# Kernel tuning notes

Measured on AMD Instinct MI355X. Metric: run time of the kernel, lower is better.

The kernel has to match this reference:

```python
import jax, jax.numpy as jnp
import numpy as np

CODEBOOK_SIZE = 512
LATENT_DIM = 12
BATCH = 512
TOKENS = 256


def setup_inputs() -> dict:
    key = jax.random.key(0)
    k1, k2 = jax.random.split(key)
    x = jax.random.normal(k1, (BATCH, TOKENS, LATENT_DIM), dtype=jnp.float32)
    # nn.Embedding init: uniform(-1/K, 1/K)
    lim = 1.0 / CODEBOOK_SIZE
    codebook = jax.random.uniform(k2, (CODEBOOK_SIZE, LATENT_DIM), dtype=jnp.float32,
                                  minval=-lim, maxval=lim)
    return {"x": x, "codebook": codebook}


def reference(x, codebook):
    # same as for torch.cdist (sqrt is monotonic).
    x2 = jnp.sum(x * x, axis=-1, keepdims=True)            # [B, N, 1]
    w2 = jnp.sum(codebook * codebook, axis=-1)             # [K]
    xw = jnp.einsum('bnd,kd->bnk', x, codebook)            # [B, N, K]
    dist2 = x2 - 2.0 * xw + w2                             # [B, N, K]
    indices = jnp.argmin(dist2, axis=-1)                   # [B, N] int
    quantized = codebook[indices]                          # [B, N, D]

    codebook_loss = jnp.mean((quantized - jax.lax.stop_gradient(x)) ** 2)
    commitment_loss = 0.25 * jnp.mean((jax.lax.stop_gradient(quantized) - x) ** 2)
    quantize_loss = codebook_loss + commitment_loss

    # straight-through estimator
    quantized_st = x + jax.lax.stop_gradient(quantized - x)
    return quantized_st, indices, quantize_loss
```

## Files before the change

### kernel.cpp

```cpp
#include <hip/hip_runtime.h>
#include <math.h>

namespace {
constexpr int KCB   = 512;
constexpr int DIM   = 12;
constexpr int NTOK  = 512 * 256;
constexpr int QSIZE = NTOK * DIM;
constexpr int CPL   = 8;
constexpr int TPW   = 32;
constexpr int NWAVE = NTOK / TPW;
constexpr float LSCALE = 1.25f / (float)QSIZE;

__global__ __launch_bounds__(256, 3) void vq_main(const float* __restrict__ x,
                                                  const float* __restrict__ cb,
                                                  float* __restrict__ out,
                                                  float* __restrict__ partials) {
    const int tid  = threadIdx.x;
    const int lane = tid & 63;
    const int wv   = __builtin_amdgcn_readfirstlane(tid >> 6);
    const int wgid = blockIdx.x * 4 + wv;
    const int tb   = wgid * TPW;

    float cw[CPL][DIM];
    float w2[CPL];
#pragma unroll
    for (int j = 0; j < CPL; ++j) {
        const float4* cr = (const float4*)(cb + (size_t)(j * 64 + lane) * DIM);
        float4 c0 = cr[0], c1 = cr[1], c2 = cr[2];
        cw[j][0] = c0.x; cw[j][1] = c0.y; cw[j][2]  = c0.z; cw[j][3]  = c0.w;
        cw[j][4] = c1.x; cw[j][5] = c1.y; cw[j][6]  = c1.z; cw[j][7]  = c1.w;
        cw[j][8] = c2.x; cw[j][9] = c2.y; cw[j][10] = c2.z; cw[j][11] = c2.w;
        float t2 = 0.f;
#pragma unroll
        for (int d = 0; d < DIM; ++d) t2 = fmaf(cw[j][d], cw[j][d], t2);
        w2[j] = t2;
    }

    float losssum = 0.f;
    float idxbuf  = 0.f;

    for (int t = 0; t < TPW; ++t) {
        const float* xr = x + (size_t)(tb + t) * DIM;
        float4 a0 = *(const float4*)(xr + 0);
        float4 a1 = *(const float4*)(xr + 4);
        float4 a2 = *(const float4*)(xr + 8);
        float xv[DIM] = {a0.x, a0.y, a0.z, a0.w, a1.x, a1.y, a1.z, a1.w,
                         a2.x, a2.y, a2.z, a2.w};
        float x2 = 0.f;
#pragma unroll
        for (int d = 0; d < DIM; ++d) x2 = fmaf(xv[d], xv[d], x2);

        float best = INFINITY;
        int   bidx = 0;
        int   kk   = lane;
#pragma unroll
        for (int j = 0; j < CPL; ++j) {
            float xw = 0.f;
            xw = fmaf(xv[0],  cw[j][0],  xw);
            xw = fmaf(xv[1],  cw[j][1],  xw);
            xw = fmaf(xv[2],  cw[j][2],  xw);
            xw = fmaf(xv[3],  cw[j][3],  xw);
            xw = fmaf(xv[4],  cw[j][4],  xw);
            xw = fmaf(xv[5],  cw[j][5],  xw);
            xw = fmaf(xv[6],  cw[j][6],  xw);
            xw = fmaf(xv[7],  cw[j][7],  xw);
            xw = fmaf(xv[8],  cw[j][8],  xw);
            xw = fmaf(xv[9],  cw[j][9],  xw);
            xw = fmaf(xv[10], cw[j][10], xw);
            xw = fmaf(xv[11], cw[j][11], xw);
            float dsc = fmaf(-2.f, xw, x2) + w2[j];
            bool c = dsc < best;
            best = c ? dsc : best;
            bidx = c ? kk : bidx;
            kk += 64;
        }

        float smin = best;
#pragma unroll
        for (int off = 1; off < 64; off <<= 1)
            smin = fminf(smin, __shfl_xor(smin, off));

        unsigned long long mask = __ballot(best == smin);
        int widx;
        if (mask & (mask - 1)) {
            int cand = (best == smin) ? bidx : 0x7fffffff;
#pragma unroll
            for (int off = 1; off < 64; off <<= 1) {
                int o = __shfl_xor(cand, off);
                cand = o < cand ? o : cand;
            }
            widx = cand;
        } else {
            widx = __builtin_amdgcn_readlane(bidx, (int)__builtin_ctzll(mask));
        }

        idxbuf  = (lane == t) ? (float)widx : idxbuf;
        losssum = fmaf(smin, LSCALE, losssum);
    }

    if (lane < TPW) {
        const int t   = tb + lane;
        const int bid = (int)idxbuf;
        const float4* xp = (const float4*)(x + (size_t)t * DIM);
        float4 a0 = xp[0], a1 = xp[1], a2 = xp[2];
        const float4* wr = (const float4*)(cb + (size_t)bid * DIM);
        float4 q0 = wr[0], q1 = wr[1], q2 = wr[2];
        float4 r0, r1, r2;
        r0.x = a0.x + (q0.x - a0.x); r0.y = a0.y + (q0.y - a0.y);
        r0.z = a0.z + (q0.z - a0.z); r0.w = a0.w + (q0.w - a0.w);
        r1.x = a1.x + (q1.x - a1.x); r1.y = a1.y + (q1.y - a1.y);
        r1.z = a1.z + (q1.z - a1.z); r1.w = a1.w + (q1.w - a1.w);
        r2.x = a2.x + (q2.x - a2.x); r2.y = a2.y + (q2.y - a2.y);
        r2.z = a2.z + (q2.z - a2.z); r2.w = a2.w + (q2.w - a2.w);
        float4* qo = (float4*)(out + (size_t)t * DIM);
        qo[0] = r0; qo[1] = r1; qo[2] = r2;
        out[QSIZE + t] = (float)bid;
    }
    if (lane == 0) partials[wgid] = losssum;
}

__global__ __launch_bounds__(1024) void reduce_loss(const float* __restrict__ p,
                                                    float* __restrict__ out) {
    float v = (p[threadIdx.x] + p[threadIdx.x + 1024]) +
              (p[threadIdx.x + 2048] + p[threadIdx.x + 3072]);
#pragma unroll
    for (int off = 32; off > 0; off >>= 1) v += __shfl_down(v, off);
    __shared__ float r[16];
    if ((threadIdx.x & 63) == 0) r[threadIdx.x >> 6] = v;
    __syncthreads();
    if (threadIdx.x == 0) {
        float s = 0.f;
#pragma unroll
        for (int i = 0; i < 16; ++i) s += r[i];
        out[QSIZE + NTOK] = s;
    }
}
}

extern "C" void kernel_launch(void* const* d_in, const int* in_sizes, int n_in,
                              void* d_out, int out_size, void* d_ws, size_t ws_size,
                              hipStream_t stream) {
    const float* x  = (const float*)d_in[0];
    const float* cb = (const float*)d_in[1];
    float* out = (float*)d_out;
    float* partials = (float*)d_ws;

    vq_main<<<NWAVE / 4, 256, 0, stream>>>(x, cb, out, partials);
    reduce_loss<<<1, 1024, 0, stream>>>(partials, out);
}
```

Measured before the change: 104.8 us.

## Compute codebook distances with split-bf16 MFMA and exact fp32 rescan for near-ties

Replaces the per-lane fp32 FMA distance loop with bf16 MFMA 16x16x32 instructions. Each operand is split into high and low bf16 parts so the dot product keeps close to fp32 accuracy. A pre-pass packs the codebook fragments and norms into the workspace, and the main kernel tracks the best and second-best distance per token. Tokens whose gap falls under an epsilon are appended to a list through an atomic counter and recomputed exactly in fp32 by a rescan kernel. This trades FMA work for matrix-core throughput, at the cost of two extra launches, an atomic, and a correctness risk if the epsilon is too tight.

New measurement: 165.6 us. 58.1% more time.

```diff
diff --git a/kernel.cpp b/kernel.cpp
--- a/kernel.cpp
+++ b/kernel.cpp
@@ -2,121 +2,280 @@
 #include <math.h>
 
 namespace {
+typedef __attribute__((ext_vector_type(8))) short bf16x8;
+typedef __attribute__((ext_vector_type(4))) float f32x4;
+
 constexpr int KCB   = 512;
 constexpr int DIM   = 12;
 constexpr int NTOK  = 512 * 256;
 constexpr int QSIZE = NTOK * DIM;
-constexpr int CPL   = 8;
-constexpr int TPW   = 32;
-constexpr int NWAVE = NTOK / TPW;
+constexpr int NTILE = KCB / 16;
+constexpr int WAVES = 4096;
+constexpr int NBLK  = WAVES / 8;
 constexpr float LSCALE = 1.25f / (float)QSIZE;
-
-__global__ __launch_bounds__(256, 3) void vq_main(const float* __restrict__ x,
+constexpr float EPS = 4e-5f;
+
+__device__ inline unsigned short bf16_rne(float f) {
+    unsigned u = __float_as_uint(f);
+    unsigned r = u + 0x7fffu + ((u >> 16) & 1u);
+    return (unsigned short)(r >> 16);
+}
+__device__ inline float bf16f(unsigned short h) {
+    return __uint_as_float(((unsigned)h) << 16);
+}
+
+__global__ __launch_bounds__(256) void pack_frags(const float* __restrict__ cb,
+                                                  uint4* __restrict__ wtab,
+                                                  float* __restrict__ w2s,
+                                                  int* __restrict__ counter) {
+    int g = blockIdx.x * 256 + threadIdx.x;
+    if (g == 0) *counter = 0;
+    if (g >= NTILE * 64) return;
+    int lane = g & 63, q = lane >> 4;
+    int n = (g >> 6) * 16 + (lane & 15);
+    float w[DIM];
+#pragma unroll
+    for (int d = 0; d < DIM; ++d) w[d] = cb[n * DIM + d];
+    unsigned short h[DIM], l[DIM];
+#pragma unroll
+    for (int d = 0; d < DIM; ++d) {
+        h[d] = bf16_rne(w[d]);
+        l[d] = bf16_rne(w[d] - bf16f(h[d]));
+    }
+    unsigned short s1[8], s2[8];
+#pragma unroll
+    for (int j = 0; j < 8; ++j) {
+        int k = q * 8 + j;
+        s1[j] = (k < 12) ? h[k] : (k < 24 ? h[k - 12] : (unsigned short)0);
+        s2[j] = (k < 12) ? l[k] : (k < 24 ? l[k - 12] : (unsigned short)0);
+    }
+    uint4 v1, v2;
+    v1.x = s1[0] | ((unsigned)s1[1] << 16); v1.y = s1[2] | ((unsigned)s1[3] << 16);
+    v1.z = s1[4] | ((unsigned)s1[5] << 16); v1.w = s1[6] | ((unsigned)s1[7] << 16);
+    v2.x = s2[0] | ((unsigned)s2[1] << 16); v2.y = s2[2] | ((unsigned)s2[3] << 16);
+    v2.z = s2[4] | ((unsigned)s2[5] << 16); v2.w = s2[6] | ((unsigned)s2[7] << 16);
+    wtab[g] = v1;
+    wtab[2048 + g] = v2;
+    if (q == 0) {
+        float w2 = 0.f;
+#pragma unroll
+        for (int d = 0; d < DIM; ++d) w2 = fmaf(w[d], w[d], w2);
+        w2s[n] = w2;
+    }
+}
+
+__global__ __launch_bounds__(512, 2) void vq_mfma(const float* __restrict__ x,
                                                   const float* __restrict__ cb,
+                                                  const uint4* __restrict__ wtab,
+                                                  const float* __restrict__ w2s,
                                                   float* __restrict__ out,
-                                                  float* __restrict__ partials) {
+                                                  float* __restrict__ partials,
+                                                  int* __restrict__ counter,
+                                                  int* __restrict__ list) {
+    __shared__ uint4 lds[4096];
     const int tid  = threadIdx.x;
     const int lane = tid & 63;
     const int wv   = __builtin_amdgcn_readfirstlane(tid >> 6);
-    const int wgid = blockIdx.x * 4 + wv;
-    const int tb   = wgid * TPW;
-
-    float cw[CPL][DIM];
-    float w2[CPL];
-#pragma unroll
-    for (int j = 0; j < CPL; ++j) {
-        const float4* cr = (const float4*)(cb + (size_t)(j * 64 + lane) * DIM);
-        float4 c0 = cr[0], c1 = cr[1], c2 = cr[2];
-        cw[j][0] = c0.x; cw[j][1] = c0.y; cw[j][2]  = c0.z; cw[j][3]  = c0.w;
-        cw[j][4] = c1.x; cw[j][5] = c1.y; cw[j][6]  = c1.z; cw[j][7]  = c1.w;
-        cw[j][8] = c2.x; cw[j][9] = c2.y; cw[j][10] = c2.z; cw[j][11] = c2.w;
-        float t2 = 0.f;
-#pragma unroll
-        for (int d = 0; d < DIM; ++d) t2 = fmaf(cw[j][d], cw[j][d], t2);
-        w2[j] = t2;
-    }
-
-    float losssum = 0.f;
-    float idxbuf  = 0.f;
-
-    for (int t = 0; t < TPW; ++t) {
-        const float* xr = x + (size_t)(tb + t) * DIM;
-        float4 a0 = *(const float4*)(xr + 0);
-        float4 a1 = *(const float4*)(xr + 4);
-        float4 a2 = *(const float4*)(xr + 8);
+    const int wgid = blockIdx.x * 8 + wv;
+    const int Mb   = wgid * 2;
+    const int m    = lane & 15;
+    const int q    = lane >> 4;
+
+    for (int i = tid; i < 4096; i += 512) lds[i] = wtab[i];
+
+    bf16x8 A[2];
+    float x2own[2];
+#pragma unroll
+    for (int i = 0; i < 2; ++i) {
+        const float4* xr = (const float4*)(x + (size_t)((Mb + i) * 16 + m) * DIM);
+        float4 a0 = xr[0], a1 = xr[1], a2 = xr[2];
         float xv[DIM] = {a0.x, a0.y, a0.z, a0.w, a1.x, a1.y, a1.z, a1.w,
                          a2.x, a2.y, a2.z, a2.w};
+        float t2 = 0.f;
+#pragma unroll
+        for (int d = 0; d < DIM; ++d) t2 = fmaf(xv[d], xv[d], t2);
+        x2own[i] = t2;
+        unsigned short h[DIM], l[DIM];
+#pragma unroll
+        for (int d = 0; d < DIM; ++d) {
+            h[d] = bf16_rne(xv[d]);
+            l[d] = bf16_rne(xv[d] - bf16f(h[d]));
+        }
+        unsigned short s[8];
+        if (q == 0) {
+#pragma unroll
+            for (int j = 0; j < 8; ++j) s[j] = h[j];
+        } else if (q == 1) {
+            s[0] = h[8]; s[1] = h[9]; s[2] = h[10]; s[3] = h[11];
+            s[4] = l[0]; s[5] = l[1]; s[6] = l[2];  s[7] = l[3];
+        } else if (q == 2) {
+#pragma unroll
+            for (int j = 0; j < 8; ++j) s[j] = l[j + 4];
+        } else {
+#pragma unroll
+            for (int j = 0; j < 8; ++j) s[j] = 0;
+        }
+#pragma unroll
+        for (int j = 0; j < 8; ++j) A[i][j] = (short)s[j];
+    }
+    float x2r[2][4];
+#pragma unroll
+    for (int i = 0; i < 2; ++i)
+#pragma unroll
+        for (int r = 0; r < 4; ++r) x2r[i][r] = __shfl(x2own[i], q * 4 + r);
+
+    __syncthreads();
+
+    float m1[2][4], m2[2][4];
+    int   bI[2][4];
+#pragma unroll
+    for (int i = 0; i < 2; ++i)
+#pragma unroll
+        for (int r = 0; r < 4; ++r) { m1[i][r] = INFINITY; m2[i][r] = INFINITY; bI[i][r] = 0; }
+
+    const float* w2p = w2s + m;
+#pragma unroll 2
+    for (int t = 0; t < NTILE; ++t) {
+        uint4 b1 = lds[t * 64 + lane];
+        uint4 b2 = lds[2048 + t * 64 + lane];
+        bf16x8 B1 = __builtin_bit_cast(bf16x8, b1);
+        bf16x8 B2 = __builtin_bit_cast(bf16x8, b2);
+        float w2c = w2p[t * 16];
+        f32x4 C0 = {0.f, 0.f, 0.f, 0.f};
+        C0 = __builtin_amdgcn_mfma_f32_16x16x32_bf16(A[0], B1, C0, 0, 0, 0);
+        C0 = __builtin_amdgcn_mfma_f32_16x16x32_bf16(A[0], B2, C0, 0, 0, 0);
+        f32x4 C1 = {0.f, 0.f, 0.f, 0.f};
+        C1 = __builtin_amdgcn_mfma_f32_16x16x32_bf16(A[1], B1, C1, 0, 0, 0);
+        C1 = __builtin_amdgcn_mfma_f32_16x16x32_bf16(A[1], B2, C1, 0, 0, 0);
+        const int idxc = t * 16 + m;
+#pragma unroll
+        for (int r = 0; r < 4; ++r) {
+            float s0 = fmaf(-2.f, C0[r], x2r[0][r]) + w2c;
+            m2[0][r] = fminf(m2[0][r], fmaxf(m1[0][r], s0));
+            bool c0 = s0 < m1[0][r];
+            m1[0][r] = c0 ? s0 : m1[0][r];
+            bI[0][r] = c0 ? idxc : bI[0][r];
+            float s1 = fmaf(-2.f, C1[r], x2r[1][r]) + w2c;
+            m2[1][r] = fminf(m2[1][r], fmaxf(m1[1][r], s1));
+            bool c1 = s1 < m1[1][r];
+            m1[1][r] = c1 ? s1 : m1[1][r];
+            bI[1][r] = c1 ? idxc : bI[1][r];
+        }
+    }
+
+    unsigned long long keyf[2][4];
+    float m1f[2][4], m2f[2][4];
+#pragma unroll
+    for (int i = 0; i < 2; ++i)
+#pragma unroll
+        for (int r = 0; r < 4; ++r) {
+            unsigned su = __float_as_uint(m1[i][r]);
+            su = (su & 0x80000000u) ? ~su : (su | 0x80000000u);
+            unsigned long long k = ((unsigned long long)su << 32) | (unsigned)bI[i][r];
+            float a1 = m1[i][r], a2 = m2[i][r];
+#pragma unroll
+            for (int off = 1; off < 16; off <<= 1) {
+                unsigned long long ko = __shfl_xor(k, off);
+                float b1v = __shfl_xor(a1, off);
+                float b2v = __shfl_xor(a2, off);
+                a2 = fminf(fminf(a2, b2v), fmaxf(a1, b1v));
+                a1 = fminf(a1, b1v);
+                k  = ko < k ? ko : k;
+            }
+            keyf[i][r] = k; m1f[i][r] = a1; m2f[i][r] = a2;
+        }
+
+    float lossacc = 0.f;
+    if (m < 4) {
+#pragma unroll
+        for (int i = 0; i < 2; ++i) {
+            unsigned long long kk = (m == 0) ? keyf[i][0] : (m == 1) ? keyf[i][1]
+                                  : (m == 2) ? keyf[i][2] : keyf[i][3];
+            float s1v = (m == 0) ? m1f[i][0] : (m == 1) ? m1f[i][1]
+                      : (m == 2) ? m1f[i][2] : m1f[i][3];
+            float s2v = (m == 0) ? m2f[i][0] : (m == 1) ? m2f[i][1]
+                      : (m == 2) ? m2f[i][2] : m2f[i][3];
+            const int bid = (int)(kk & 0xffffffffULL);
+            const int t = (Mb + i) * 16 + q * 4 + m;
+            const float4* xp = (const float4*)(x + (size_t)t * DIM);
+            float4 a0 = xp[0], a1 = xp[1], a2 = xp[2];
+            const float4* wr = (const float4*)(cb + (size_t)bid * DIM);
+            float4 q0 = wr[0], q1 = wr[1], q2 = wr[2];
+            float4 r0, r1, r2;
+            r0.x = a0.x + (q0.x - a0.x); r0.y = a0.y + (q0.y - a0.y);
+            r0.z = a0.z + (q0.z - a0.z); r0.w = a0.w + (q0.w - a0.w);
+            r1.x = a1.x + (q1.x - a1.x); r1.y = a1.y + (q1.y - a1.y);
+            r1.z = a1.z + (q1.z - a1.z); r1.w = a1.w + (q1.w - a1.w);
+            r2.x = a2.x + (q2.x - a2.x); r2.y = a2.y + (q2.y - a2.y);
+            r2.z = a2.z + (q2.z - a2.z); r2.w = a2.w + (q2.w - a2.w);
+            float4* qo = (float4*)(out + (size_t)t * DIM);
+            qo[0] = r0; qo[1] = r1; qo[2] = r2;
+            out[QSIZE + t] = (float)bid;
+            lossacc += s1v;
+            if (s2v - s1v <= EPS) {
+                int slot = atomicAdd(counter, 1);
+                list[slot] = t;
+            }
+        }
+    }
+    lossacc *= LSCALE;
+#pragma unroll
+    for (int off = 32; off > 0; off >>= 1) lossacc += __shfl_down(lossacc, off);
+    if (lane == 0) partials[wgid] = lossacc;
+}
+
+__global__ __launch_bounds__(256) void rescan(const float* __restrict__ x,
+                                              const float* __restrict__ cb,
+                                              const float* __restrict__ w2s,
+                                              float* __restrict__ out,
+                                              const int* __restrict__ counter,
+                                              const int* __restrict__ list) {
+    const int n = *counter;
+    for (int i = blockIdx.x * 256 + threadIdx.x; i < n; i += gridDim.x * 256) {
+        const int t = list[i];
+        const float4* xp = (const float4*)(x + (size_t)t * DIM);
+        float4 a0 = xp[0], a1 = xp[1], a2 = xp[2];
+        float xs[DIM] = {a0.x, a0.y, a0.z, a0.w, a1.x, a1.y, a1.z, a1.w,
+                         a2.x, a2.y, a2.z, a2.w};
         float x2 = 0.f;
 #pragma unroll
-        for (int d = 0; d < DIM; ++d) x2 = fmaf(xv[d], xv[d], x2);
-
+        for (int d = 0; d < DIM; ++d) x2 = fmaf(xs[d], xs[d], x2);
         float best = INFINITY;
-        int   bidx = 0;
-        int   kk   = lane;
-#pragma unroll
-        for (int j = 0; j < CPL; ++j) {
+        int bi = 0;
+        for (int k = 0; k < KCB; ++k) {
+            const float4* cr = (const float4*)(cb + (size_t)k * DIM);
+            float4 c0 = cr[0], c1 = cr[1], c2 = cr[2];
             float xw = 0.f;
-            xw = fmaf(xv[0],  cw[j][0],  xw);
-            xw = fmaf(xv[1],  cw[j][1],  xw);
-            xw = fmaf(xv[2],  cw[j][2],  xw);
-            xw = fmaf(xv[3],  cw[j][3],  xw);
-            xw = fmaf(xv[4],  cw[j][4],  xw);
-            xw = fmaf(xv[5],  cw[j][5],  xw);
-            xw = fmaf(xv[6],  cw[j][6],  xw);
-            xw = fmaf(xv[7],  cw[j][7],  xw);
-            xw = fmaf(xv[8],  cw[j][8],  xw);
-            xw = fmaf(xv[9],  cw[j][9],  xw);
-            xw = fmaf(xv[10], cw[j][10], xw);
-            xw = fmaf(xv[11], cw[j][11], xw);
-            float dsc = fmaf(-2.f, xw, x2) + w2[j];
+            xw = fmaf(xs[0],  c0.x, xw);
+            xw = fmaf(xs[1],  c0.y, xw);
+            xw = fmaf(xs[2],  c0.z, xw);
+            xw = fmaf(xs[3],  c0.w, xw);
+            xw = fmaf(xs[4],  c1.x, xw);
+            xw = fmaf(xs[5],  c1.y, xw);
+            xw = fmaf(xs[6],  c1.z, xw);
+            xw = fmaf(xs[7],  c1.w, xw);
+            xw = fmaf(xs[8],  c2.x, xw);
+            xw = fmaf(xs[9],  c2.y, xw);
+            xw = fmaf(xs[10], c2.z, xw);
+            xw = fmaf(xs[11], c2.w, xw);
+            float dsc = fmaf(-2.f, xw, x2) + w2s[k];
             bool c = dsc < best;
             best = c ? dsc : best;
-            bidx = c ? kk : bidx;
-            kk += 64;
-        }
-
-        float smin = best;
-#pragma unroll
-        for (int off = 1; off < 64; off <<= 1)
-            smin = fminf(smin, __shfl_xor(smin, off));
-
-        unsigned long long mask = __ballot(best == smin);
-        int widx;
-        if (mask & (mask - 1)) {
-            int cand = (best == smin) ? bidx : 0x7fffffff;
-#pragma unroll
-            for (int off = 1; off < 64; off <<= 1) {
-                int o = __shfl_xor(cand, off);
-                cand = o < cand ? o : cand;
-            }
-            widx = cand;
-        } else {
-            widx = __builtin_amdgcn_readlane(bidx, (int)__builtin_ctzll(mask));
-        }
-
-        idxbuf  = (lane == t) ? (float)widx : idxbuf;
-        losssum = fmaf(smin, LSCALE, losssum);
-    }
-
-    if (lane < TPW) {
-        const int t   = tb + lane;
-        const int bid = (int)idxbuf;
-        const float4* xp = (const float4*)(x + (size_t)t * DIM);
-        float4 a0 = xp[0], a1 = xp[1], a2 = xp[2];
-        const float4* wr = (const float4*)(cb + (size_t)bid * DIM);
+            bi   = c ? k : bi;
+        }
+        const float4* wr = (const float4*)(cb + (size_t)bi * DIM);
         float4 q0 = wr[0], q1 = wr[1], q2 = wr[2];
         float4 r0, r1, r2;
-        r0.x = a0.x + (q0.x - a0.x); r0.y = a0.y + (q0.y - a0.y);
-        r0.z = a0.z + (q0.z - a0.z); r0.w = a0.w + (q0.w - a0.w);
-        r1.x = a1.x + (q1.x - a1.x); r1.y = a1.y + (q1.y - a1.y);
-        r1.z = a1.z + (q1.z - a1.z); r1.w = a1.w + (q1.w - a1.w);
-        r2.x = a2.x + (q2.x - a2.x); r2.y = a2.y + (q2.y - a2.y);
-        r2.z = a2.z + (q2.z - a2.z); r2.w = a2.w + (q2.w - a2.w);
+        r0.x = xs[0] + (q0.x - xs[0]);   r0.y = xs[1] + (q0.y - xs[1]);
+        r0.z = xs[2] + (q0.z - xs[2]);   r0.w = xs[3] + (q0.w - xs[3]);
+        r1.x = xs[4] + (q1.x - xs[4]);   r1.y = xs[5] + (q1.y - xs[5]);
+        r1.z = xs[6] + (q1.z - xs[6]);   r1.w = xs[7] + (q1.w - xs[7]);
+        r2.x = xs[8] + (q2.x - xs[8]);   r2.y = xs[9] + (q2.y - xs[9]);
+        r2.z = xs[10] + (q2.z - xs[10]); r2.w = xs[11] + (q2.w - xs[11]);
         float4* qo = (float4*)(out + (size_t)t * DIM);
         qo[0] = r0; qo[1] = r1; qo[2] = r2;
-        out[QSIZE + t] = (float)bid;
-    }
-    if (lane == 0) partials[wgid] = losssum;
+        out[QSIZE + t] = (float)bi;
+    }
 }
 
 __global__ __launch_bounds__(1024) void reduce_loss(const float* __restrict__ p,
@@ -143,8 +302,15 @@
     const float* x  = (const float*)d_in[0];
     const float* cb = (const float*)d_in[1];
     float* out = (float*)d_out;
-    float* partials = (float*)d_ws;
-
-    vq_main<<<NWAVE / 4, 256, 0, stream>>>(x, cb, out, partials);
+    char* ws = (char*)d_ws;
+    uint4* wtab     = (uint4*)ws;
+    float* w2s      = (float*)(ws + 65536);
+    int*   counter  = (int*)(ws + 67584);
+    int*   list     = (int*)(ws + 69632);
+    float* partials = (float*)(ws + 655360);
+
+    pack_frags<<<8, 256, 0, stream>>>(cb, wtab, w2s, counter);
+    vq_mfma<<<NBLK, 512, 0, stream>>>(x, cb, wtab, w2s, out, partials, counter, list);
+    rescan<<<128, 256, 0, stream>>>(x, cb, w2s, out, counter, list);
     reduce_loss<<<1, 1024, 0, stream>>>(partials, out);
 }
```
